# Kernel tuning notes

Hardware: AMD Instinct MI355X
Metric: run time of the kernel (lower is better)

## Reference

```python
import jax, jax.numpy as jnp
import numpy as np

LN_EPS = 1e-5
ATTN_THRESH = 0.0005


def _layernorm(x, g, b):
    mu = jnp.mean(x, axis=-1, keepdims=True)
    var = jnp.mean((x - mu) ** 2, axis=-1, keepdims=True)
    return (x - mu) / jnp.sqrt(var + LN_EPS) * g + b


def setup_inputs() -> dict:
    key = jax.random.key(0)
    ks = jax.random.split(key, 10)
    B, P, X, C = 4, 1024, 8192, 1024
    return {
        "feat": jax.random.normal(ks[0], (B, P, C), dtype=jnp.float32),
        "mem_k": jax.random.normal(ks[1], (B, X, C), dtype=jnp.float32),
        "mem_v": jax.random.normal(ks[2], (B, X, C), dtype=jnp.float32),
        "mem_c": jax.random.uniform(ks[3], (B, X, 1), dtype=jnp.float32),
        "mem_attn": jnp.zeros((B, X, 1), dtype=jnp.float32),
        "g_q": jax.random.uniform(ks[4], (C,), dtype=jnp.float32, minval=0.5, maxval=1.5),
        "b_q": jax.random.normal(ks[5], (C,), dtype=jnp.float32) * 0.02,
        "g_k": jax.random.uniform(ks[6], (C,), dtype=jnp.float32, minval=0.5, maxval=1.5),
        "b_k": jax.random.normal(ks[7], (C,), dtype=jnp.float32) * 0.02,
        "g_v": jax.random.uniform(ks[8], (C,), dtype=jnp.float32, minval=0.5, maxval=1.5),
        "b_v": jax.random.normal(ks[9], (C,), dtype=jnp.float32) * 0.02,
    }


def reference(feat, mem_k, mem_v, mem_c, mem_attn, g_q, b_q, g_k, b_k, g_v, b_v):
    # SpatialMemory.memory_read with res=True
    C = feat.shape[-1]
    q = _layernorm(feat, g_q, b_q)                      # [B,P,C]
    k = _layernorm(mem_k, g_k, b_k)                     # [B,X,C]
    affinity = jnp.einsum('bpc,bxc->bpx', q, k)
    affinity = affinity / jnp.sqrt(jnp.asarray(C, jnp.float32))
    # confidence scaling: mem_c viewed as [B,1,X]
    affinity = affinity * jnp.swapaxes(mem_c, 1, 2)
    attn = jax.nn.softmax(affinity, axis=-1)            # [B,P,X]
    # threshold sparsify + renormalize
    attn = jnp.where(attn < ATTN_THRESH, jnp.zeros((), attn.dtype), attn)
    attn = attn / jnp.sum(attn, axis=-1, keepdims=True)
    v = _layernorm(mem_v, g_v, b_v)                     # [B,X,C]
    out = jnp.einsum('bpx,bxc->bpc', attn, v) + feat    # residual
    return out
```

## Files before the change

kernel.cpp:

```cpp
#include <hip/hip_runtime.h>

typedef __attribute__((ext_vector_type(8))) _Float16 half8;
typedef __attribute__((ext_vector_type(4))) _Float16 half4v;
typedef __attribute__((ext_vector_type(4))) float f32x4;

__device__ __forceinline__ void gll16(const void* g, void* l) {
  __builtin_amdgcn_global_load_lds(
      (const __attribute__((address_space(1))) unsigned int*)g,
      (__attribute__((address_space(3))) unsigned int*)l, 16, 0, 0);
}

__device__ __forceinline__ float h2f(unsigned short hb) {
  _Float16 h;
  __builtin_memcpy(&h, &hb, 2);
  return (float)h;
}

__global__ __launch_bounds__(256) void ln_cast_f16(
    const float* __restrict__ x, const float* __restrict__ g,
    const float* __restrict__ b, _Float16* __restrict__ y) {
  const int C = 1024;
  size_t row = blockIdx.x;
  int t = threadIdx.x;
  const float4* xr = (const float4*)(x + row * C);
  float4 v = xr[t];
  float s = v.x + v.y + v.z + v.w;
  float s2 = v.x * v.x + v.y * v.y + v.z * v.z + v.w * v.w;
#pragma unroll
  for (int off = 1; off < 64; off <<= 1) {
    s += __shfl_xor(s, off, 64);
    s2 += __shfl_xor(s2, off, 64);
  }
  __shared__ float ps[4], ps2[4];
  int wave = t >> 6, lane = t & 63;
  if (lane == 0) { ps[wave] = s; ps2[wave] = s2; }
  __syncthreads();
  s = ps[0] + ps[1] + ps[2] + ps[3];
  s2 = ps2[0] + ps2[1] + ps2[2] + ps2[3];
  float mu = s * (1.0f / C);
  float var = s2 * (1.0f / C) - mu * mu;
  float rstd = rsqrtf(var + 1e-5f);
  float4 gv = ((const float4*)g)[t];
  float4 bv = ((const float4*)b)[t];
  half4v o;
  o.x = (_Float16)((v.x - mu) * rstd * gv.x + bv.x);
  o.y = (_Float16)((v.y - mu) * rstd * gv.y + bv.y);
  o.z = (_Float16)((v.z - mu) * rstd * gv.z + bv.z);
  o.w = (_Float16)((v.w - mu) * rstd * gv.w + bv.w);
  ((half4v*)(y + row * C))[t] = o;
}

__global__ __launch_bounds__(256) void ln_cast_i8(
    const float* __restrict__ x, const float* __restrict__ g,
    const float* __restrict__ b, char* __restrict__ y,
    float* __restrict__ yscale) {
  const int C = 1024;
  size_t row = blockIdx.x;
  int t = threadIdx.x;
  const float4* xr = (const float4*)(x + row * C);
  float4 v = xr[t];
  float s = v.x + v.y + v.z + v.w;
  float s2 = v.x * v.x + v.y * v.y + v.z * v.z + v.w * v.w;
#pragma unroll
  for (int off = 1; off < 64; off <<= 1) {
    s += __shfl_xor(s, off, 64);
    s2 += __shfl_xor(s2, off, 64);
  }
  __shared__ float ps[4], ps2[4], pm[4];
  int wave = t >> 6, lane = t & 63;
  if (lane == 0) { ps[wave] = s; ps2[wave] = s2; }
  __syncthreads();
  s = ps[0] + ps[1] + ps[2] + ps[3];
  s2 = ps2[0] + ps2[1] + ps2[2] + ps2[3];
  float mu = s * (1.0f / C);
  float var = s2 * (1.0f / C) - mu * mu;
  float rstd = rsqrtf(var + 1e-5f);
  float4 gv = ((const float4*)g)[t];
  float4 bv = ((const float4*)b)[t];
  float o0 = (v.x - mu) * rstd * gv.x + bv.x;
  float o1 = (v.y - mu) * rstd * gv.y + bv.y;
  float o2 = (v.z - mu) * rstd * gv.z + bv.z;
  float o3 = (v.w - mu) * rstd * gv.w + bv.w;
  float mx = fmaxf(fmaxf(fabsf(o0), fabsf(o1)), fmaxf(fabsf(o2), fabsf(o3)));
#pragma unroll
  for (int off = 1; off < 64; off <<= 1) mx = fmaxf(mx, __shfl_xor(mx, off, 64));
  if (lane == 0) pm[wave] = mx;
  __syncthreads();
  mx = fmaxf(fmaxf(pm[0], pm[1]), fmaxf(pm[2], pm[3]));
  mx = fmaxf(mx, 1e-20f);
  float inv = 127.0f / mx;
  int q0 = (int)rintf(o0 * inv), q1 = (int)rintf(o1 * inv);
  int q2 = (int)rintf(o2 * inv), q3 = (int)rintf(o3 * inv);
  unsigned pk = ((unsigned)(q0 & 0xff)) | ((unsigned)(q1 & 0xff) << 8) |
                ((unsigned)(q2 & 0xff) << 16) | ((unsigned)(q3 & 0xff) << 24);
  ((unsigned*)(y + row * C))[t] = pk;
  if (t == 0) yscale[row] = mx * (1.0f / 127.0f);
}

__global__ __launch_bounds__(256) void gemm_qk_pipe(
    const _Float16* __restrict__ A,
    const _Float16* __restrict__ Bm,
    _Float16* __restrict__ Sm,
    const float* __restrict__ conf)
{
  const int N = 8192, K = 1024, NSTG = 32;
  int bz = blockIdx.z;
  const _Float16* Ab = A + (size_t)bz * 1024 * K;
  const _Float16* Bb = Bm + (size_t)bz * (size_t)N * K;
  _Float16* Sb = Sm + (size_t)bz * 1024 * N;

  __shared__ _Float16 lA[3 * 4096];
  __shared__ _Float16 lB[3 * 4096];

  int tid = threadIdx.x;
  int wave = tid >> 6, lane = tid & 63;
  int wm = wave >> 1, wn = wave & 1;
  int m0 = blockIdx.y * 128, n0 = blockIdx.x * 128;

  f32x4 acc[4][4];
  f32x4 zero = {0.f, 0.f, 0.f, 0.f};
#pragma unroll
  for (int i = 0; i < 4; ++i)
#pragma unroll
    for (int j = 0; j < 4; ++j) acc[i][j] = zero;

  int rS = tid & 127, kg0 = tid >> 7, kg1 = kg0 + 2;
  const _Float16* gA0 = Ab + (size_t)(m0 + rS) * K + kg0 * 8;
  const _Float16* gA1 = Ab + (size_t)(m0 + rS) * K + kg1 * 8;
  const _Float16* gB0 = Bb + (size_t)(n0 + rS) * K + kg0 * 8;
  const _Float16* gB1 = Bb + (size_t)(n0 + rS) * K + kg1 * 8;
  int d0 = kg0 * 1024 + rS * 8;
  int d1 = kg1 * 1024 + rS * 8;

  gll16(gA0, &lA[d0]); gll16(gA1, &lA[d1]);
  gll16(gB0, &lB[d0]); gll16(gB1, &lB[d1]);
  gll16(gA0 + 32, &lA[4096 + d0]); gll16(gA1 + 32, &lA[4096 + d1]);
  gll16(gB0 + 32, &lB[4096 + d0]); gll16(gB1 + 32, &lB[4096 + d1]);

  int kg = lane >> 4, lr = lane & 15;
  int bfc = 0;
  int bfi = 2;

  for (int k = 0; k < NSTG; ++k) {
    if (k <= NSTG - 3)
      __builtin_amdgcn_s_waitcnt(0xF74);
    else
      __builtin_amdgcn_s_waitcnt(0xF70);
    __builtin_amdgcn_s_barrier();
    __builtin_amdgcn_sched_barrier(0);
    if (k <= NSTG - 3) {
      int kk = (k + 2) * 32;
      int bo = bfi * 4096;
      gll16(gA0 + kk, &lA[bo + d0]); gll16(gA1 + kk, &lA[bo + d1]);
      gll16(gB0 + kk, &lB[bo + d0]); gll16(gB1 + kk, &lB[bo + d1]);
    }
    const _Float16* la = &lA[bfc * 4096];
    const _Float16* lb = &lB[bfc * 4096];
    half8 af[4], bfr[4];
#pragma unroll
    for (int t = 0; t < 4; ++t) {
      af[t] = *(const half8*)&la[kg * 1024 + (wm * 64 + t * 16 + lr) * 8];
      bfr[t] = *(const half8*)&lb[kg * 1024 + (wn * 64 + t * 16 + lr) * 8];
    }
#pragma unroll
    for (int t = 0; t < 4; ++t)
#pragma unroll
      for (int u = 0; u < 4; ++u)
        acc[t][u] = __builtin_amdgcn_mfma_f32_16x16x32_f16(af[t], bfr[u], acc[t][u], 0, 0, 0);
    __builtin_amdgcn_sched_barrier(0);
    bfc = (bfc == 2) ? 0 : bfc + 1;
    bfi = (bfi == 2) ? 0 : bfi + 1;
  }

  int cq = lane >> 4, cn = lane & 15;
  const float* cb = conf + (size_t)bz * N;
#pragma unroll
  for (int u = 0; u < 4; ++u) {
    int gn = n0 + wn * 64 + u * 16 + cn;
    float cs = 0.03125f * cb[gn];
#pragma unroll
    for (int t = 0; t < 4; ++t) {
      int gm = m0 + wm * 64 + t * 16 + cq * 4;
#pragma unroll
      for (int r = 0; r < 4; ++r)
        Sb[(size_t)(gm + r) * N + gn] = (_Float16)(acc[t][u][r] * cs);
    }
  }
}

__global__ __launch_bounds__(256) void softmax_compact(
    const _Float16* __restrict__ S, unsigned* __restrict__ entries,
    int* __restrict__ counts) {
  const int X = 8192;
  size_t row = blockIdx.x;
  const half8* sr = (const half8*)(S + row * X);
  int t = threadIdx.x;
  int wave = t >> 6, lane = t & 63;
  __shared__ float sh[4];
  __shared__ int scnt;

  float v[32];
#pragma unroll
  for (int j = 0; j < 4; ++j) {
    half8 h = sr[t + j * 256];
#pragma unroll
    for (int c = 0; c < 8; ++c) v[j * 8 + c] = (float)h[c];
  }

  float m = -1e30f;
#pragma unroll
  for (int i = 0; i < 32; ++i) m = fmaxf(m, v[i]);
#pragma unroll
  for (int off = 1; off < 64; off <<= 1) m = fmaxf(m, __shfl_xor(m, off, 64));
  if (lane == 0) sh[wave] = m;
  __syncthreads();
  m = fmaxf(fmaxf(sh[0], sh[1]), fmaxf(sh[2], sh[3]));
  __syncthreads();

  float l = 0.f;
#pragma unroll
  for (int i = 0; i < 32; ++i) {
    v[i] = __expf(v[i] - m);
    l += v[i];
  }
#pragma unroll
  for (int off = 1; off < 64; off <<= 1) l += __shfl_xor(l, off, 64);
  if (lane == 0) sh[wave] = l;
  __syncthreads();
  l = sh[0] + sh[1] + sh[2] + sh[3];
  __syncthreads();

  float thr = 0.0005f * l;
  float ks = 0.f;
#pragma unroll
  for (int i = 0; i < 32; ++i) {
    v[i] = (v[i] >= thr) ? v[i] : 0.f;
    ks += v[i];
  }
#pragma unroll
  for (int off = 1; off < 64; off <<= 1) ks += __shfl_xor(ks, off, 64);
  if (lane == 0) sh[wave] = ks;
  __syncthreads();
  if (t == 0) scnt = 0;
  __syncthreads();
  ks = sh[0] + sh[1] + sh[2] + sh[3];

  float inv = 1.0f / ks;
  unsigned* er = entries + row * 2048;
#pragma unroll
  for (int j = 0; j < 4; ++j) {
#pragma unroll
    for (int c = 0; c < 8; ++c) {
      float val = v[j * 8 + c];
      if (val > 0.f) {
        int pos = atomicAdd(&scnt, 1);
        _Float16 h = (_Float16)(val * inv);
        unsigned short hb;
        __builtin_memcpy(&hb, &h, 2);
        er[pos] = ((unsigned)((t + j * 256) * 8 + c) << 16) | hb;
      }
    }
  }
  __syncthreads();
  if (t == 0) counts[row] = scnt;
}

__device__ __forceinline__ void acc4(float* a, unsigned w, float wt) {
  a[0] += wt * (float)(signed char)(w & 0xff);
  a[1] += wt * (float)(signed char)((w >> 8) & 0xff);
  a[2] += wt * (float)(signed char)((w >> 16) & 0xff);
  a[3] += wt * (float)(signed char)(w >> 24);
}

__global__ __launch_bounds__(512) void gather_pv_i8(
    const unsigned* __restrict__ entries, const int* __restrict__ counts,
    const char* __restrict__ v8, const float* __restrict__ vscale,
    const float* __restrict__ feat, float* __restrict__ out) {
  const int X = 8192, C = 1024;
  int row = blockIdx.x;
  int b = row >> 10;
  int t = threadIdx.x;
  int s = t >> 6;
  int lane = t & 63;
  int c = lane * 16;

  __shared__ unsigned se[2048];
  __shared__ float red[8][1028];

  int cnt = counts[row];
  const unsigned* er = entries + (size_t)row * 2048;
  for (int i = t; i < cnt; i += 512) se[i] = er[i];
  __syncthreads();

  const char* vb = v8 + (size_t)b * X * C;
  const float* sb = vscale + (size_t)b * X;
  float a[16];
#pragma unroll
  for (int i = 0; i < 16; ++i) a[i] = 0.f;

#pragma unroll 2
  for (int j = s; j < cnt; j += 8) {
    unsigned e = se[j];
    int x = e >> 16;
    float w = h2f((unsigned short)(e & 0xffff)) * sb[x];
    uint4 pv = *(const uint4*)(vb + (size_t)x * C + c);
    acc4(a + 0, pv.x, w);
    acc4(a + 4, pv.y, w);
    acc4(a + 8, pv.z, w);
    acc4(a + 12, pv.w, w);
  }
  float* rp = &red[s][c];
#pragma unroll
  for (int i = 0; i < 16; ++i) rp[i] = a[i];
  __syncthreads();

  int p = t * 2;
  float2 f = *(const float2*)(feat + (size_t)row * C + p);
  float o0 = f.x, o1 = f.y;
#pragma unroll
  for (int ss = 0; ss < 8; ++ss) {
    o0 += red[ss][p];
    o1 += red[ss][p + 1];
  }
  float2 o = {o0, o1};
  *(float2*)(out + (size_t)row * C + p) = o;
}

extern "C" void kernel_launch(void* const* d_in, const int* in_sizes, int n_in,
                              void* d_out, int out_size, void* d_ws, size_t ws_size,
                              hipStream_t stream) {
  const int B = 4, P = 1024, X = 8192, C = 1024;
  const float* feat  = (const float*)d_in[0];
  const float* mem_k = (const float*)d_in[1];
  const float* mem_v = (const float*)d_in[2];
  const float* mem_c = (const float*)d_in[3];
  const float* g_q = (const float*)d_in[5];
  const float* b_q = (const float*)d_in[6];
  const float* g_k = (const float*)d_in[7];
  const float* b_k = (const float*)d_in[8];
  const float* g_v = (const float*)d_in[9];
  const float* b_v = (const float*)d_in[10];

  char* ws = (char*)d_ws;
  const size_t MB = 1024 * 1024;
  _Float16* q16 = (_Float16*)(ws + 0);
  _Float16* k16 = (_Float16*)(ws + 8 * MB);
  _Float16* S   = (_Float16*)(ws + 72 * MB);
  char*     v8  = (char*)(ws + 136 * MB);
  float* vscale = (float*)(ws + 168 * MB);
  unsigned* entries = (unsigned*)(ws + 169 * MB);
  int*      counts  = (int*)(ws + 201 * MB);

  ln_cast_f16<<<B * P, 256, 0, stream>>>(feat, g_q, b_q, q16);
  ln_cast_f16<<<B * X, 256, 0, stream>>>(mem_k, g_k, b_k, k16);
  ln_cast_i8<<<B * X, 256, 0, stream>>>(mem_v, g_v, b_v, v8, vscale);
  gemm_qk_pipe<<<dim3(X / 128, P / 128, B), 256, 0, stream>>>(q16, k16, S, mem_c);
  softmax_compact<<<B * P, 256, 0, stream>>>(S, entries, counts);
  gather_pv_i8<<<B * P, 512, 0, stream>>>(entries, counts, v8, vscale, feat,
                                          (float*)d_out);
}
```

Baseline: 527.6 us.

## Enlarge QK GEMM tile to 256x256 with 32x32 MFMA and 4-stage pipeline

Replaces the 128x128 QK^T GEMM (256 threads, 16x16x32 MFMA, 3-buffer LDS ring) with a 256x256 tile on 512 threads using 32x32x16 MFMA, a 4-deep LDS ring, and setprio around the MFMA bursts. Larger tiles raise arithmetic intensity and cut global/LDS traffic per FLOP, and the bigger MFMA shape lowers instruction-issue overhead. In exchange it uses 128KB of LDS per block, adds a second barrier per K step, and produces far fewer blocks. That can limit occupancy, and the strided fp16 epilogue stores may scatter.

```diff
diff --git a/kernel.cpp b/kernel.cpp
--- a/kernel.cpp
+++ b/kernel.cpp
@@ -3,6 +3,7 @@
 typedef __attribute__((ext_vector_type(8))) _Float16 half8;
 typedef __attribute__((ext_vector_type(4))) _Float16 half4v;
 typedef __attribute__((ext_vector_type(4))) float f32x4;
+typedef __attribute__((ext_vector_type(16))) float f32x16;
 
 __device__ __forceinline__ void gll16(const void* g, void* l) {
   __builtin_amdgcn_global_load_lds(
@@ -97,93 +98,118 @@
   if (t == 0) yscale[row] = mx * (1.0f / 127.0f);
 }
 
-__global__ __launch_bounds__(256) void gemm_qk_pipe(
+__global__ __launch_bounds__(512, 2) void gemm_qk_256(
     const _Float16* __restrict__ A,
     const _Float16* __restrict__ Bm,
     _Float16* __restrict__ Sm,
     const float* __restrict__ conf)
 {
-  const int N = 8192, K = 1024, NSTG = 32;
+  const int N = 8192, K = 1024;
   int bz = blockIdx.z;
   const _Float16* Ab = A + (size_t)bz * 1024 * K;
   const _Float16* Bb = Bm + (size_t)bz * (size_t)N * K;
   _Float16* Sb = Sm + (size_t)bz * 1024 * N;
 
-  __shared__ _Float16 lA[3 * 4096];
-  __shared__ _Float16 lB[3 * 4096];
+  __shared__ _Float16 lA[4 * 8192];
+  __shared__ _Float16 lB[4 * 8192];
 
   int tid = threadIdx.x;
   int wave = tid >> 6, lane = tid & 63;
-  int wm = wave >> 1, wn = wave & 1;
-  int m0 = blockIdx.y * 128, n0 = blockIdx.x * 128;
-
-  f32x4 acc[4][4];
-  f32x4 zero = {0.f, 0.f, 0.f, 0.f};
+  int wm = wave >> 2, wn = wave & 3;
+  int lr = lane & 31, lk = lane >> 5;
+  int m0 = blockIdx.y * 256, n0 = blockIdx.x * 256;
+
+  f32x16 acc[4][2];
 #pragma unroll
   for (int i = 0; i < 4; ++i)
 #pragma unroll
-    for (int j = 0; j < 4; ++j) acc[i][j] = zero;
-
-  int rS = tid & 127, kg0 = tid >> 7, kg1 = kg0 + 2;
-  const _Float16* gA0 = Ab + (size_t)(m0 + rS) * K + kg0 * 8;
-  const _Float16* gA1 = Ab + (size_t)(m0 + rS) * K + kg1 * 8;
-  const _Float16* gB0 = Bb + (size_t)(n0 + rS) * K + kg0 * 8;
-  const _Float16* gB1 = Bb + (size_t)(n0 + rS) * K + kg1 * 8;
-  int d0 = kg0 * 1024 + rS * 8;
-  int d1 = kg1 * 1024 + rS * 8;
-
-  gll16(gA0, &lA[d0]); gll16(gA1, &lA[d1]);
-  gll16(gB0, &lB[d0]); gll16(gB1, &lB[d1]);
-  gll16(gA0 + 32, &lA[4096 + d0]); gll16(gA1 + 32, &lA[4096 + d1]);
-  gll16(gB0 + 32, &lB[4096 + d0]); gll16(gB1 + 32, &lB[4096 + d1]);
-
-  int kg = lane >> 4, lr = lane & 15;
-  int bfc = 0;
-  int bfi = 2;
-
-  for (int k = 0; k < NSTG; ++k) {
-    if (k <= NSTG - 3)
-      __builtin_amdgcn_s_waitcnt(0xF74);
-    else
-      __builtin_amdgcn_s_waitcnt(0xF70);
+    for (int j = 0; j < 2; ++j)
+#pragma unroll
+      for (int e = 0; e < 16; ++e) acc[i][j][e] = 0.f;
+
+  int r = tid & 255, c0 = tid >> 8;
+  const _Float16* gA = Ab + (size_t)(m0 + r) * K + c0 * 8;
+  const _Float16* gB = Bb + (size_t)(n0 + r) * K + c0 * 8;
+  int dA = c0 * 2048 + r * 8;
+
+  auto stage = [&](int t) {
+    int bo = (t & 3) * 8192;
+    const _Float16* ga = gA + t * 32;
+    const _Float16* gb = gB + t * 32;
+    gll16(ga, &lA[bo + dA]);
+    gll16(ga + 16, &lA[bo + dA + 4096]);
+    gll16(gb, &lB[bo + dA]);
+    gll16(gb + 16, &lB[bo + dA + 4096]);
+  };
+
+  auto compute = [&](int bo) {
+#pragma unroll
+    for (int ks = 0; ks < 2; ++ks) {
+      const _Float16* la = &lA[bo + (ks * 2 + lk) * 2048 + (wm * 128 + lr) * 8];
+      const _Float16* lb = &lB[bo + (ks * 2 + lk) * 2048 + (wn * 64 + lr) * 8];
+      half8 a0 = *(const half8*)(la);
+      half8 a1 = *(const half8*)(la + 256);
+      half8 a2 = *(const half8*)(la + 512);
+      half8 a3 = *(const half8*)(la + 768);
+      half8 b0 = *(const half8*)(lb);
+      half8 b1 = *(const half8*)(lb + 256);
+      __builtin_amdgcn_s_setprio(1);
+      acc[0][0] = __builtin_amdgcn_mfma_f32_32x32x16_f16(a0, b0, acc[0][0], 0, 0, 0);
+      acc[1][0] = __builtin_amdgcn_mfma_f32_32x32x16_f16(a1, b0, acc[1][0], 0, 0, 0);
+      acc[2][0] = __builtin_amdgcn_mfma_f32_32x32x16_f16(a2, b0, acc[2][0], 0, 0, 0);
+      acc[3][0] = __builtin_amdgcn_mfma_f32_32x32x16_f16(a3, b0, acc[3][0], 0, 0, 0);
+      acc[0][1] = __builtin_amdgcn_mfma_f32_32x32x16_f16(a0, b1, acc[0][1], 0, 0, 0);
+      acc[1][1] = __builtin_amdgcn_mfma_f32_32x32x16_f16(a1, b1, acc[1][1], 0, 0, 0);
+      acc[2][1] = __builtin_amdgcn_mfma_f32_32x32x16_f16(a2, b1, acc[2][1], 0, 0, 0);
+      acc[3][1] = __builtin_amdgcn_mfma_f32_32x32x16_f16(a3, b1, acc[3][1], 0, 0, 0);
+      __builtin_amdgcn_s_setprio(0);
+    }
+  };
+
+  stage(0);
+  stage(1);
+  stage(2);
+
+#pragma unroll 4
+  for (int kt = 0; kt < 29; ++kt) {
+    stage(kt + 3);
+    __builtin_amdgcn_s_waitcnt(0xF7C);
     __builtin_amdgcn_s_barrier();
     __builtin_amdgcn_sched_barrier(0);
-    if (k <= NSTG - 3) {
-      int kk = (k + 2) * 32;
-      int bo = bfi * 4096;
-      gll16(gA0 + kk, &lA[bo + d0]); gll16(gA1 + kk, &lA[bo + d1]);
-      gll16(gB0 + kk, &lB[bo + d0]); gll16(gB1 + kk, &lB[bo + d1]);
-    }
-    const _Float16* la = &lA[bfc * 4096];
-    const _Float16* lb = &lB[bfc * 4096];
-    half8 af[4], bfr[4];
-#pragma unroll
-    for (int t = 0; t < 4; ++t) {
-      af[t] = *(const half8*)&la[kg * 1024 + (wm * 64 + t * 16 + lr) * 8];
-      bfr[t] = *(const half8*)&lb[kg * 1024 + (wn * 64 + t * 16 + lr) * 8];
-    }
-#pragma unroll
-    for (int t = 0; t < 4; ++t)
-#pragma unroll
-      for (int u = 0; u < 4; ++u)
-        acc[t][u] = __builtin_amdgcn_mfma_f32_16x16x32_f16(af[t], bfr[u], acc[t][u], 0, 0, 0);
+    compute((kt & 3) * 8192);
     __builtin_amdgcn_sched_barrier(0);
-    bfc = (bfc == 2) ? 0 : bfc + 1;
-    bfi = (bfi == 2) ? 0 : bfi + 1;
-  }
-
-  int cq = lane >> 4, cn = lane & 15;
+    __builtin_amdgcn_s_barrier();
+  }
+  __builtin_amdgcn_s_waitcnt(0xF78);
+  __builtin_amdgcn_s_barrier();
+  __builtin_amdgcn_sched_barrier(0);
+  compute(1 * 8192);
+  __builtin_amdgcn_sched_barrier(0);
+  __builtin_amdgcn_s_barrier();
+  __builtin_amdgcn_s_waitcnt(0xF74);
+  __builtin_amdgcn_s_barrier();
+  __builtin_amdgcn_sched_barrier(0);
+  compute(2 * 8192);
+  __builtin_amdgcn_sched_barrier(0);
+  __builtin_amdgcn_s_barrier();
+  __builtin_amdgcn_s_waitcnt(0xF70);
+  __builtin_amdgcn_s_barrier();
+  __builtin_amdgcn_sched_barrier(0);
+  compute(3 * 8192);
+
   const float* cb = conf + (size_t)bz * N;
 #pragma unroll
-  for (int u = 0; u < 4; ++u) {
-    int gn = n0 + wn * 64 + u * 16 + cn;
+  for (int nf = 0; nf < 2; ++nf) {
+    int gn = n0 + wn * 64 + nf * 32 + lr;
     float cs = 0.03125f * cb[gn];
 #pragma unroll
-    for (int t = 0; t < 4; ++t) {
-      int gm = m0 + wm * 64 + t * 16 + cq * 4;
-#pragma unroll
-      for (int r = 0; r < 4; ++r)
-        Sb[(size_t)(gm + r) * N + gn] = (_Float16)(acc[t][u][r] * cs);
+    for (int mf = 0; mf < 4; ++mf) {
+      int gmb = m0 + wm * 128 + mf * 32 + 4 * lk;
+#pragma unroll
+      for (int rr = 0; rr < 16; ++rr) {
+        int gm = gmb + (rr & 3) + 8 * (rr >> 2);
+        Sb[(size_t)gm * N + gn] = (_Float16)(acc[mf][nf][rr] * cs);
+      }
     }
   }
 }
@@ -354,7 +380,7 @@
   ln_cast_f16<<<B * P, 256, 0, stream>>>(feat, g_q, b_q, q16);
   ln_cast_f16<<<B * X, 256, 0, stream>>>(mem_k, g_k, b_k, k16);
   ln_cast_i8<<<B * X, 256, 0, stream>>>(mem_v, g_v, b_v, v8, vscale);
-  gemm_qk_pipe<<<dim3(X / 128, P / 128, B), 256, 0, stream>>>(q16, k16, S, mem_c);
+  gemm_qk_256<<<dim3(X / 256, P / 256, B), 512, 0, stream>>>(q16, k16, S, mem_c);
   softmax_compact<<<B * P, 256, 0, stream>>>(S, entries, counts);
   gather_pv_i8<<<B * P, 512, 0, stream>>>(entries, counts, v8, vscale, feat,
                                           (float*)d_out);
```

Measured after the change: 504.1 us. -4.5%, faster.

## Rewrite QK GEMM with 256x256 tiles, 8 waves and phased ping-pong pipeline

Applied to the files above, without the earlier changes.

Replaces the 128x128 triple-buffered QK^T GEMM with a 256x256 tile computed by 512 threads (8 waves, each 128x64), double-buffered over 64-wide K chunks. Each K chunk runs as four phases that interleave LDS reads, async global-to-LDS loads for the next chunk, and 16-MFMA bursts at raised wave priority. The aim is more operand reuse per LDS byte and better overlap of loads with matrix math. In exchange it needs 128 KB of LDS per block and many more accumulator registers, which limits occupancy, and a 1024x8192 problem per batch yields fewer blocks, which may hurt load balance across CUs.

```diff
diff --git a/kernel.cpp b/kernel.cpp
--- a/kernel.cpp
+++ b/kernel.cpp
@@ -97,93 +97,130 @@
   if (t == 0) yscale[row] = mx * (1.0f / 127.0f);
 }
 
-__global__ __launch_bounds__(256) void gemm_qk_pipe(
+__global__ __launch_bounds__(512, 2) void gemm_qk_8ph(
     const _Float16* __restrict__ A,
     const _Float16* __restrict__ Bm,
     _Float16* __restrict__ Sm,
     const float* __restrict__ conf)
 {
-  const int N = 8192, K = 1024, NSTG = 32;
+  const int N = 8192, K = 1024;
   int bz = blockIdx.z;
   const _Float16* Ab = A + (size_t)bz * 1024 * K;
   const _Float16* Bb = Bm + (size_t)bz * (size_t)N * K;
   _Float16* Sb = Sm + (size_t)bz * 1024 * N;
 
-  __shared__ _Float16 lA[3 * 4096];
-  __shared__ _Float16 lB[3 * 4096];
+  __shared__ _Float16 lA[2 * 16384];
+  __shared__ _Float16 lB[2 * 16384];
 
   int tid = threadIdx.x;
   int wave = tid >> 6, lane = tid & 63;
-  int wm = wave >> 1, wn = wave & 1;
-  int m0 = blockIdx.y * 128, n0 = blockIdx.x * 128;
-
-  f32x4 acc[4][4];
-  f32x4 zero = {0.f, 0.f, 0.f, 0.f};
-#pragma unroll
-  for (int i = 0; i < 4; ++i)
-#pragma unroll
-    for (int j = 0; j < 4; ++j) acc[i][j] = zero;
-
-  int rS = tid & 127, kg0 = tid >> 7, kg1 = kg0 + 2;
-  const _Float16* gA0 = Ab + (size_t)(m0 + rS) * K + kg0 * 8;
-  const _Float16* gA1 = Ab + (size_t)(m0 + rS) * K + kg1 * 8;
-  const _Float16* gB0 = Bb + (size_t)(n0 + rS) * K + kg0 * 8;
-  const _Float16* gB1 = Bb + (size_t)(n0 + rS) * K + kg1 * 8;
-  int d0 = kg0 * 1024 + rS * 8;
-  int d1 = kg1 * 1024 + rS * 8;
-
-  gll16(gA0, &lA[d0]); gll16(gA1, &lA[d1]);
-  gll16(gB0, &lB[d0]); gll16(gB1, &lB[d1]);
-  gll16(gA0 + 32, &lA[4096 + d0]); gll16(gA1 + 32, &lA[4096 + d1]);
-  gll16(gB0 + 32, &lB[4096 + d0]); gll16(gB1 + 32, &lB[4096 + d1]);
-
-  int kg = lane >> 4, lr = lane & 15;
-  int bfc = 0;
-  int bfi = 2;
-
-  for (int k = 0; k < NSTG; ++k) {
-    if (k <= NSTG - 3)
-      __builtin_amdgcn_s_waitcnt(0xF74);
-    else
-      __builtin_amdgcn_s_waitcnt(0xF70);
-    __builtin_amdgcn_s_barrier();
-    __builtin_amdgcn_sched_barrier(0);
-    if (k <= NSTG - 3) {
-      int kk = (k + 2) * 32;
-      int bo = bfi * 4096;
-      gll16(gA0 + kk, &lA[bo + d0]); gll16(gA1 + kk, &lA[bo + d1]);
-      gll16(gB0 + kk, &lB[bo + d0]); gll16(gB1 + kk, &lB[bo + d1]);
+  int wm = wave >> 2, wn = wave & 3;
+  int lr16 = lane & 15, lq = lane >> 4;
+  int m0 = blockIdx.y * 256, n0 = blockIdx.x * 256;
+
+  f32x4 acc[8][4];
+#pragma unroll
+  for (int i = 0; i < 8; ++i)
+#pragma unroll
+    for (int j = 0; j < 4; ++j) {
+      f32x4 z = {0.f, 0.f, 0.f, 0.f};
+      acc[i][j] = z;
     }
-    const _Float16* la = &lA[bfc * 4096];
-    const _Float16* lb = &lB[bfc * 4096];
-    half8 af[4], bfr[4];
-#pragma unroll
-    for (int t = 0; t < 4; ++t) {
-      af[t] = *(const half8*)&la[kg * 1024 + (wm * 64 + t * 16 + lr) * 8];
-      bfr[t] = *(const half8*)&lb[kg * 1024 + (wn * 64 + t * 16 + lr) * 8];
+  half8 bfr[4];
+
+  int r = tid & 255, c0 = tid >> 8;
+  const _Float16* gA = Ab + (size_t)(m0 + r) * K;
+  const _Float16* gB = Bb + (size_t)(n0 + r) * K;
+  int ldst = r * 8;
+
+  auto stage_half = [&](int t, int h) {
+    int kb = t * 64 + h * 32;
+    int bo = (t & 1) * 16384;
+#pragma unroll
+    for (int j = 0; j < 2; ++j) {
+      int c = c0 + 2 * j;
+      gll16(gA + kb + c * 8, &lA[bo + (h * 4 + c) * 2048 + ldst]);
+      gll16(gB + kb + c * 8, &lB[bo + (h * 4 + c) * 2048 + ldst]);
     }
-#pragma unroll
-    for (int t = 0; t < 4; ++t)
-#pragma unroll
-      for (int u = 0; u < 4; ++u)
-        acc[t][u] = __builtin_amdgcn_mfma_f32_16x16x32_f16(af[t], bfr[u], acc[t][u], 0, 0, 0);
-    __builtin_amdgcn_sched_barrier(0);
-    bfc = (bfc == 2) ? 0 : bfc + 1;
-    bfi = (bfi == 2) ? 0 : bfi + 1;
-  }
-
-  int cq = lane >> 4, cn = lane & 15;
+  };
+
+#define DO_PHASE(BO, MH, KS, READB, STAGE_STMT, WAIT_STMT)                        \
+  {                                                                               \
+    __builtin_amdgcn_sched_barrier(0);                                            \
+    const _Float16* la_ =                                                         \
+        &lA[(BO) + ((KS)*4 + lq) * 2048 + (wm * 128 + (MH)*64 + lr16) * 8];       \
+    half8 a0_ = *(const half8*)(la_);                                             \
+    half8 a1_ = *(const half8*)(la_ + 128);                                       \
+    half8 a2_ = *(const half8*)(la_ + 256);                                       \
+    half8 a3_ = *(const half8*)(la_ + 384);                                       \
+    if (READB) {                                                                  \
+      const _Float16* lb_ =                                                       \
+          &lB[(BO) + ((KS)*4 + lq) * 2048 + (wn * 64 + lr16) * 8];                \
+      bfr[0] = *(const half8*)(lb_);                                              \
+      bfr[1] = *(const half8*)(lb_ + 128);                                        \
+      bfr[2] = *(const half8*)(lb_ + 256);                                        \
+      bfr[3] = *(const half8*)(lb_ + 384);                                        \
+    }                                                                             \
+    STAGE_STMT;                                                                   \
+    __builtin_amdgcn_sched_barrier(0);                                            \
+    __builtin_amdgcn_s_barrier();                                                 \
+    __builtin_amdgcn_sched_barrier(0);                                            \
+    __builtin_amdgcn_s_setprio(1);                                                \
+    acc[(MH)*4 + 0][0] = __builtin_amdgcn_mfma_f32_16x16x32_f16(a0_, bfr[0], acc[(MH)*4 + 0][0], 0, 0, 0); \
+    acc[(MH)*4 + 0][1] = __builtin_amdgcn_mfma_f32_16x16x32_f16(a0_, bfr[1], acc[(MH)*4 + 0][1], 0, 0, 0); \
+    acc[(MH)*4 + 0][2] = __builtin_amdgcn_mfma_f32_16x16x32_f16(a0_, bfr[2], acc[(MH)*4 + 0][2], 0, 0, 0); \
+    acc[(MH)*4 + 0][3] = __builtin_amdgcn_mfma_f32_16x16x32_f16(a0_, bfr[3], acc[(MH)*4 + 0][3], 0, 0, 0); \
+    acc[(MH)*4 + 1][0] = __builtin_amdgcn_mfma_f32_16x16x32_f16(a1_, bfr[0], acc[(MH)*4 + 1][0], 0, 0, 0); \
+    acc[(MH)*4 + 1][1] = __builtin_amdgcn_mfma_f32_16x16x32_f16(a1_, bfr[1], acc[(MH)*4 + 1][1], 0, 0, 0); \
+    acc[(MH)*4 + 1][2] = __builtin_amdgcn_mfma_f32_16x16x32_f16(a1_, bfr[2], acc[(MH)*4 + 1][2], 0, 0, 0); \
+    acc[(MH)*4 + 1][3] = __builtin_amdgcn_mfma_f32_16x16x32_f16(a1_, bfr[3], acc[(MH)*4 + 1][3], 0, 0, 0); \
+    acc[(MH)*4 + 2][0] = __builtin_amdgcn_mfma_f32_16x16x32_f16(a2_, bfr[0], acc[(MH)*4 + 2][0], 0, 0, 0); \
+    acc[(MH)*4 + 2][1] = __builtin_amdgcn_mfma_f32_16x16x32_f16(a2_, bfr[1], acc[(MH)*4 + 2][1], 0, 0, 0); \
+    acc[(MH)*4 + 2][2] = __builtin_amdgcn_mfma_f32_16x16x32_f16(a2_, bfr[2], acc[(MH)*4 + 2][2], 0, 0, 0); \
+    acc[(MH)*4 + 2][3] = __builtin_amdgcn_mfma_f32_16x16x32_f16(a2_, bfr[3], acc[(MH)*4 + 2][3], 0, 0, 0); \
+    acc[(MH)*4 + 3][0] = __builtin_amdgcn_mfma_f32_16x16x32_f16(a3_, bfr[0], acc[(MH)*4 + 3][0], 0, 0, 0); \
+    acc[(MH)*4 + 3][1] = __builtin_amdgcn_mfma_f32_16x16x32_f16(a3_, bfr[1], acc[(MH)*4 + 3][1], 0, 0, 0); \
+    acc[(MH)*4 + 3][2] = __builtin_amdgcn_mfma_f32_16x16x32_f16(a3_, bfr[2], acc[(MH)*4 + 3][2], 0, 0, 0); \
+    acc[(MH)*4 + 3][3] = __builtin_amdgcn_mfma_f32_16x16x32_f16(a3_, bfr[3], acc[(MH)*4 + 3][3], 0, 0, 0); \
+    __builtin_amdgcn_s_setprio(0);                                                \
+    __builtin_amdgcn_sched_barrier(0);                                            \
+    WAIT_STMT;                                                                    \
+    __builtin_amdgcn_s_barrier();                                                 \
+  }
+
+  stage_half(0, 0);
+  stage_half(0, 1);
+  __builtin_amdgcn_s_waitcnt(0xF74);
+  __builtin_amdgcn_s_barrier();
+
+#pragma unroll 1
+  for (int t = 0; t < 15; ++t) {
+    int bo = (t & 1) * 16384;
+    DO_PHASE(bo, 0, 0, true,  (stage_half(t + 1, 0)), ((void)0));
+    DO_PHASE(bo, 1, 0, false, ((void)0), __builtin_amdgcn_s_waitcnt(0xF74));
+    DO_PHASE(bo, 0, 1, true,  (stage_half(t + 1, 1)), ((void)0));
+    DO_PHASE(bo, 1, 1, false, ((void)0), __builtin_amdgcn_s_waitcnt(0xF74));
+  }
+  {
+    int bo = 16384;
+    DO_PHASE(bo, 0, 0, true,  ((void)0), ((void)0));
+    DO_PHASE(bo, 1, 0, false, ((void)0), __builtin_amdgcn_s_waitcnt(0xF70));
+    DO_PHASE(bo, 0, 1, true,  ((void)0), ((void)0));
+    DO_PHASE(bo, 1, 1, false, ((void)0), ((void)0));
+  }
+#undef DO_PHASE
+
   const float* cb = conf + (size_t)bz * N;
 #pragma unroll
-  for (int u = 0; u < 4; ++u) {
-    int gn = n0 + wn * 64 + u * 16 + cn;
+  for (int nf = 0; nf < 4; ++nf) {
+    int gn = n0 + wn * 64 + nf * 16 + lr16;
     float cs = 0.03125f * cb[gn];
 #pragma unroll
-    for (int t = 0; t < 4; ++t) {
-      int gm = m0 + wm * 64 + t * 16 + cq * 4;
-#pragma unroll
-      for (int r = 0; r < 4; ++r)
-        Sb[(size_t)(gm + r) * N + gn] = (_Float16)(acc[t][u][r] * cs);
+    for (int mf = 0; mf < 8; ++mf) {
+      int gm = m0 + wm * 128 + mf * 16 + lq * 4;
+#pragma unroll
+      for (int rr = 0; rr < 4; ++rr)
+        Sb[(size_t)(gm + rr) * N + gn] = (_Float16)(acc[mf][nf][rr] * cs);
     }
   }
 }
@@ -354,7 +391,7 @@
   ln_cast_f16<<<B * P, 256, 0, stream>>>(feat, g_q, b_q, q16);
   ln_cast_f16<<<B * X, 256, 0, stream>>>(mem_k, g_k, b_k, k16);
   ln_cast_i8<<<B * X, 256, 0, stream>>>(mem_v, g_v, b_v, v8, vscale);
-  gemm_qk_pipe<<<dim3(X / 128, P / 128, B), 256, 0, stream>>>(q16, k16, S, mem_c);
+  gemm_qk_8ph<<<dim3(X / 256, P / 256, B), 512, 0, stream>>>(q16, k16, S, mem_c);
   softmax_compact<<<B * P, 256, 0, stream>>>(S, entries, counts);
   gather_pv_i8<<<B * P, 512, 0, stream>>>(entries, counts, v8, vscale, feat,
                                           (float*)d_out);
```

Result: no change. 530.7 us (+0.6%).
